# Performance work log

Measured on AMD Instinct MI355X. Metric: run time of the kernel, lower is better.

## Reference

```python
import jax, jax.numpy as jnp
from jax import lax
import numpy as np

B, C, H, W = 32, 256, 16, 16          # batch, planes, feature-map HxW
NBUF, REPS, LAB = 100000, 256, 10     # buffer size, reps dim, label dim
D = REPS + LAB                        # retrieval_data feature dim
DH = 64                               # cross_dim_head (heads=1 -> inner=64)
INNER = DH
EPS = 1e-5


def _ln(x, g, b):
    m = x.mean(-1, keepdims=True)
    v = ((x - m) ** 2).mean(-1, keepdims=True)
    return (x - m) * lax.rsqrt(v + EPS) * g + b


def _conv(x, w):
    return lax.conv_general_dilated(x, w, (1, 1), 'SAME',
                                    dimension_numbers=('NCHW', 'OIHW', 'NCHW'))


def _forward(x, conv1_w, conv2_w, bn1_g, bn1_b, bn2_g, bn2_b, retrieval_data,
             ln_attn_g, ln_attn_b, ln_ctx_g, ln_ctx_b, wq, wk, wv, wqe, wo, bo,
             ln_ff_g, ln_ff_b, w1, b1, w2, b2, topk):
    # eval-mode BatchNorm with running mean=0, var=1
    bn = lambda y, g, b: y * g[None, :, None, None] + b[None, :, None, None]
    out = jax.nn.relu(bn(_conv(x, conv1_w), bn1_g, bn1_b))
    out = bn(_conv(out, conv2_w), bn2_g, bn2_b)
    out = jax.nn.relu(out + x)                        # identity shortcut
    t = out.reshape(B, C, H * W).transpose(0, 2, 1)   # [B, n, C] tokens

    # ---- retrieval cross-attention (PreNorm on x and on context) ----
    xn = _ln(t, ln_attn_g, ln_attn_b)
    ctx = _ln(retrieval_data, ln_ctx_g, ln_ctx_b)     # [NBUF, D]
    q = xn @ wq                                        # [B, n, INNER]
    emb = q @ wqe                                      # [B, n, REPS]
    e0 = emb[:, 0, :]                                  # original loop only uses position 0
    buf_reps = ctx[:, :REPS]                           # [NBUF, REPS]
    # squared L2 has the same ordering as the L2 norm used by torch.topk(largest=False)
    dist2 = jnp.sum((buf_reps[None] - e0[:, None]) ** 2, axis=-1)  # [B, NBUF]
    idx = lax.top_k(-dist2, topk)[1]                   # [B, topk] nearest indices
    retrieved = jnp.take(ctx, idx, axis=0)             # [B, topk, D]; identical for all n positions
    reps_r, labels_r = retrieved[..., :REPS], retrieved[..., REPS:]
    k = reps_r @ wk                                    # reps_for_k: K from reps  [B, topk, INNER]
    v = labels_r @ wv                                  # V from labels            [B, topk, INNER]
    sim = jnp.einsum('bnd,bjd->bnj', q, k) * DH ** -0.5
    attn = jax.nn.softmax(sim, axis=-1)
    o = jnp.einsum('bnj,bjd->bnd', attn, v)
    t = o @ wo + bo + t

    # ---- feed-forward (PreNorm, GEGLU, mult=1) ----
    h = _ln(t, ln_ff_g, ln_ff_b) @ w1 + b1             # [B, n, 2C]
    a, g = jnp.split(h, 2, axis=-1)
    t = (a * jax.nn.gelu(g, approximate=False)) @ w2 + b2 + t

    return t.transpose(0, 2, 1).reshape(B, C, H, W)


def setup_inputs() -> dict:
    key = jax.random.key(0)
    ks = jax.random.split(key, 12)
    s = 0.02
    return {
        'x': jax.random.normal(ks[0], (B, C, H, W), jnp.float32),
        'conv1_w': jax.random.normal(ks[1], (C, C, 3, 3), jnp.float32) * s,
        'conv2_w': jax.random.normal(ks[2], (C, C, 3, 3), jnp.float32) * s,
        'bn1_g': jnp.ones((C,), jnp.float32), 'bn1_b': jnp.zeros((C,), jnp.float32),
        'bn2_g': jnp.ones((C,), jnp.float32), 'bn2_b': jnp.zeros((C,), jnp.float32),
        'retrieval_data': jax.random.normal(ks[3], (NBUF, D), jnp.float32),
        'ln_attn_g': jnp.ones((C,), jnp.float32), 'ln_attn_b': jnp.zeros((C,), jnp.float32),
        'ln_ctx_g': jnp.ones((D,), jnp.float32), 'ln_ctx_b': jnp.zeros((D,), jnp.float32),
        'wq': jax.random.normal(ks[4], (C, INNER), jnp.float32) * s,
        'wk': jax.random.normal(ks[5], (REPS, INNER), jnp.float32) * s,
        'wv': jax.random.normal(ks[6], (LAB, INNER), jnp.float32) * s,
        'wqe': jax.random.normal(ks[7], (INNER, REPS), jnp.float32) * s,
        'wo': jax.random.normal(ks[8], (INNER, C), jnp.float32) * s,
        'bo': jnp.zeros((C,), jnp.float32),
        'ln_ff_g': jnp.ones((C,), jnp.float32), 'ln_ff_b': jnp.zeros((C,), jnp.float32),
        'w1': jax.random.normal(ks[9], (C, 2 * C), jnp.float32) * s,
        'b1': jnp.zeros((2 * C,), jnp.float32),
        'w2': jax.random.normal(ks[10], (C, C), jnp.float32) * s,
        'b2': jnp.zeros((C,), jnp.float32),
        'topk': 32,
    }


def reference(x, conv1_w, conv2_w, bn1_g, bn1_b, bn2_g, bn2_b, retrieval_data,
              ln_attn_g, ln_attn_b, ln_ctx_g, ln_ctx_b, wq, wk, wv, wqe, wo, bo,
              ln_ff_g, ln_ff_b, w1, b1, w2, b2, topk):
    return _forward(x, conv1_w, conv2_w, bn1_g, bn1_b, bn2_g, bn2_b, retrieval_data,
                    ln_attn_g, ln_attn_b, ln_ctx_g, ln_ctx_b, wq, wk, wv, wqe, wo, bo,
                    ln_ff_g, ln_ff_b, w1, b1, w2, b2, topk)
```

## Files before the change

### kernel.cpp

```cpp
#include <hip/hip_runtime.h>
#include <hip/hip_bf16.h>
#include <math.h>

#define DEV __device__ __forceinline__

typedef __attribute__((ext_vector_type(8))) short bf16x8;
typedef __attribute__((ext_vector_type(4))) float f32x4;
typedef __attribute__((ext_vector_type(4))) unsigned int u32x4;
typedef __attribute__((ext_vector_type(2))) unsigned int u32x2;

DEV float b2f(unsigned int u) { return __uint_as_float(u << 16); }
DEV unsigned short f2b(float f) {
    unsigned int x = __float_as_uint(f);
    unsigned int r = x + 0x7fffu + ((x >> 16) & 1u);
    return (unsigned short)(r >> 16);
}
DEV unsigned int pack2(float a, float b) {
    return (unsigned int)f2b(a) | ((unsigned int)f2b(b) << 16);
}
DEV float gelu_exact(float g) {
    return 0.5f * g * (1.f + erff(g * 0.70710678118654752f));
}

constexpr size_t WP1  = 0;
constexpr size_t WP2  = WP1  + 1179648;
constexpr size_t BPQ  = WP2  + 1179648;
constexpr size_t BPO  = BPQ  + 32768;
constexpr size_t BP1  = BPO  + 32768;
constexpr size_t BP2  = BP1  + 262144;
constexpr size_t XTP  = BP2  + 131072;
constexpr size_t O1P  = XTP  + 5308416;
constexpr size_t TBUF = O1P  + 5308416;
constexpr size_t QB   = TBUF + 8388608;
constexpr size_t E0P  = QB   + 1048576;
constexpr size_t DIST = E0P  + 16384;
constexpr size_t CANDV= DIST + 12800000;
constexpr size_t CANDI= CANDV+ 262144;
constexpr size_t IDXB = CANDI+ 262144;
constexpr size_t KBF  = IDXB + 4096;
constexpr size_t VBF  = KBF  + 262144;
constexpr size_t OBF  = VBF  + 262144;
constexpr size_t T2B  = OBF  + 1048576;
constexpr size_t XN2  = T2B  + 8388608;
constexpr size_t UBF  = XN2  + 4194304;

__global__ __launch_bounds__(256) void setup_k(
    const float* __restrict__ x, const float* __restrict__ c1w, const float* __restrict__ c2w,
    const float* __restrict__ wq, const float* __restrict__ wo,
    const float* __restrict__ w1, const float* __restrict__ w2,
    unsigned short* __restrict__ wp1, unsigned short* __restrict__ wp2,
    unsigned short* __restrict__ pq, unsigned short* __restrict__ po,
    unsigned short* __restrict__ p1, unsigned short* __restrict__ p2,
    unsigned short* __restrict__ xtp, unsigned short* __restrict__ o1p)
{
    int blk = blockIdx.x, tid = threadIdx.x;
    if (blk < 576) {
        const float* src = (blk < 288) ? c1w : c2w;
        unsigned short* dst = (blk < 288) ? wp1 : wp2;
        int f = (blk % 288) * 256 + tid;
        int lane = f & 63, s = f >> 6;
        int t = s >> 7, rem = s & 127, kc = rem >> 4, ntg = rem & 15;
        int co = ntg * 16 + (lane & 15);
        int ci0 = kc * 32 + ((lane >> 4) << 3);
        unsigned short v[8];
#pragma unroll
        for (int j = 0; j < 8; ++j) v[j] = f2b(src[((size_t)co * 256 + ci0 + j) * 9 + t]);
        u32x4 q;
        q.x = (unsigned)v[0] | ((unsigned)v[1] << 16);
        q.y = (unsigned)v[2] | ((unsigned)v[3] << 16);
        q.z = (unsigned)v[4] | ((unsigned)v[5] << 16);
        q.w = (unsigned)v[6] | ((unsigned)v[7] << 16);
        *(u32x4*)(dst + (size_t)f * 8) = q;
    } else if (blk < 688) {
        int f = (blk - 576) * 256 + tid;
        const float* src; unsigned short* dst; int NTT, lf;
        if (f < 2048)       { src = wq; dst = pq; NTT = 4;  lf = f; }
        else if (f < 4096)  { src = wo; dst = po; NTT = 16; lf = f - 2048; }
        else if (f < 20480) { src = w1; dst = p1; NTT = 32; lf = f - 4096; }
        else                { src = w2; dst = p2; NTT = 16; lf = f - 20480; }
        int lane = lf & 63, s = lf >> 6;
        int kc = s / NTT, ntg = s % NTT;
        int N = NTT * 16;
        int k0 = kc * 32 + ((lane >> 4) << 3), n = ntg * 16 + (lane & 15);
        unsigned short v[8];
#pragma unroll
        for (int j = 0; j < 8; ++j) v[j] = f2b(src[(size_t)(k0 + j) * N + n]);
        u32x4 q;
        q.x = (unsigned)v[0] | ((unsigned)v[1] << 16);
        q.y = (unsigned)v[2] | ((unsigned)v[3] << 16);
        q.z = (unsigned)v[4] | ((unsigned)v[5] << 16);
        q.w = (unsigned)v[6] | ((unsigned)v[7] << 16);
        *(u32x4*)(dst + (size_t)lf * 8) = q;
    } else {
        int img = blk - 688;
        int h = tid >> 4, w = tid & 15;
        unsigned short* dst = xtp + ((size_t)img * 324 + (h + 1) * 18 + (w + 1)) * 256;
        const float* src = x + (size_t)img * 65536 + tid;
        for (int cc = 0; cc < 8; ++cc) {
            unsigned short v[32];
#pragma unroll
            for (int j = 0; j < 32; ++j) v[j] = f2b(src[(cc * 32 + j) * 256]);
            u32x4* dp = (u32x4*)(dst + cc * 32);
#pragma unroll
            for (int i = 0; i < 4; ++i) {
                u32x4 q;
                q.x = (unsigned)v[i*8+0] | ((unsigned)v[i*8+1] << 16);
                q.y = (unsigned)v[i*8+2] | ((unsigned)v[i*8+3] << 16);
                q.z = (unsigned)v[i*8+4] | ((unsigned)v[i*8+5] << 16);
                q.w = (unsigned)v[i*8+6] | ((unsigned)v[i*8+7] << 16);
                dp[i] = q;
            }
        }
        for (int cell = tid; cell < 324; cell += 256) {
            int hh = cell / 18, ww = cell - hh * 18;
            if (hh == 0 || hh == 17 || ww == 0 || ww == 17) {
                u32x4 z = (u32x4)0u;
                u32x4* zp1 = (u32x4*)(xtp + ((size_t)img * 324 + cell) * 256);
                u32x4* zp2 = (u32x4*)(o1p + ((size_t)img * 324 + cell) * 256);
#pragma unroll
                for (int i = 0; i < 32; ++i) { zp1[i] = z; zp2[i] = z; }
            }
        }
    }
}

template<int EPI>
__global__ __launch_bounds__(256, 2) void conv_mfma(const unsigned short* __restrict__ Asrc,
                                                    const unsigned short* __restrict__ wpack,
                                                    const float* __restrict__ bng,
                                                    const float* __restrict__ bnb,
                                                    const unsigned short* __restrict__ resid,
                                                    unsigned short* __restrict__ outP,
                                                    float* __restrict__ outT)
{
    int blk = blockIdx.x;
    int img = blk >> 4, rem = blk & 15;
    int mo = rem >> 1, nh = rem & 1;
    int tid = threadIdx.x;
    int wv = tid >> 6, lane = tid & 63;
    int lq = lane >> 4, lr = lane & 15;
    int m0 = mo * 32;
    int n0 = nh * 128 + wv * 32;

    f32x4 acc[2][2];
#pragma unroll
    for (int i = 0; i < 2; ++i)
#pragma unroll
        for (int j = 0; j < 2; ++j) acc[i][j] = 0.f;

    int abase[2];
#pragma unroll
    for (int mt = 0; mt < 2; ++mt) {
        int m = m0 + mt * 16 + lr;
        int h = m >> 4, w = m & 15;
        abase[mt] = (img * 324 + (h + 1) * 18 + (w + 1)) * 256 + lq * 8;
    }
    int bb0 = (n0 >> 4) * 512 + lane * 8;

    for (int kc = 0; kc < 8; ++kc) {
#pragma unroll
        for (int tap = 0; tap < 9; ++tap) {
            int dh = tap / 3 - 1, dw = tap % 3 - 1;
            int aoff = (dh * 18 + dw) * 256 + kc * 32;
            bf16x8 a0 = *(const bf16x8*)(Asrc + abase[0] + aoff);
            bf16x8 a1 = *(const bf16x8*)(Asrc + abase[1] + aoff);
            int boff = (tap * 8 + kc) * 8192 + bb0;
            bf16x8 b0 = *(const bf16x8*)(wpack + boff);
            bf16x8 b1 = *(const bf16x8*)(wpack + boff + 512);
            acc[0][0] = __builtin_amdgcn_mfma_f32_16x16x32_bf16(a0, b0, acc[0][0], 0, 0, 0);
            acc[0][1] = __builtin_amdgcn_mfma_f32_16x16x32_bf16(a0, b1, acc[0][1], 0, 0, 0);
            acc[1][0] = __builtin_amdgcn_mfma_f32_16x16x32_bf16(a1, b0, acc[1][0], 0, 0, 0);
            acc[1][1] = __builtin_amdgcn_mfma_f32_16x16x32_bf16(a1, b1, acc[1][1], 0, 0, 0);
        }
    }
#pragma unroll
    for (int nt = 0; nt < 2; ++nt) {
        int co = n0 + nt * 16 + lr;
        float g = bng[co], bb = bnb[co];
#pragma unroll
        for (int mt = 0; mt < 2; ++mt) {
#pragma unroll
            for (int r = 0; r < 4; ++r) {
                int m = m0 + mt * 16 + lq * 4 + r;
                int h = m >> 4, w = m & 15;
                float v = acc[mt][nt][r] * g + bb;
                if (EPI == 0) {
                    v = fmaxf(v, 0.f);
                    outP[((size_t)img * 324 + (h + 1) * 18 + (w + 1)) * 256 + co] = f2b(v);
                } else {
                    v += b2f(resid[((size_t)img * 324 + (h + 1) * 18 + (w + 1)) * 256 + co]);
                    v = fmaxf(v, 0.f);
                    outT[((size_t)img * 256 + m) * 256 + co] = v;
                }
            }
        }
    }
}

__global__ __launch_bounds__(256) void lnq_k(
    const float* __restrict__ t, const float* __restrict__ g, const float* __restrict__ bta,
    const unsigned short* __restrict__ bpq, const float* __restrict__ wqe,
    unsigned short* __restrict__ qb, unsigned short* __restrict__ e0p)
{
    __shared__ __align__(16) unsigned int frag[64 * 132];
    __shared__ float qrow[64];
    int bx = blockIdx.x, tid = threadIdx.x;
    int wv = tid >> 6, lane = tid & 63;
    int c = lane * 4;
    f32x4 gv = *(const f32x4*)(g + c);
    f32x4 bv = *(const f32x4*)(bta + c);
#pragma unroll
    for (int p = 0; p < 16; ++p) {
        int rl = wv * 16 + p;
        f32x4 x = *(const f32x4*)(t + (size_t)(bx * 64 + rl) * 256 + c);
        float s  = x[0] + x[1] + x[2] + x[3];
        float ss = x[0]*x[0] + x[1]*x[1] + x[2]*x[2] + x[3]*x[3];
#pragma unroll
        for (int off = 32; off >= 1; off >>= 1) { s += __shfl_xor(s, off); ss += __shfl_xor(ss, off); }
        float mean = s * (1.f / 256.f);
        float var  = ss * (1.f / 256.f) - mean * mean;
        float rstd = rsqrtf(fmaxf(var, 0.f) + 1e-5f);
        float y0 = (x[0]-mean)*rstd*gv[0] + bv[0];
        float y1 = (x[1]-mean)*rstd*gv[1] + bv[1];
        float y2 = (x[2]-mean)*rstd*gv[2] + bv[2];
        float y3 = (x[3]-mean)*rstd*gv[3] + bv[3];
        frag[rl * 132 + 2 * lane]     = pack2(y0, y1);
        frag[rl * 132 + 2 * lane + 1] = pack2(y2, y3);
    }
    __syncthreads();
    int lq = lane >> 4, lr = lane & 15;
    f32x4 acc[4];
#pragma unroll
    for (int nt = 0; nt < 4; ++nt) acc[nt] = 0.f;
    const short* sA = (const short*)frag;
#pragma unroll
    for (int kc = 0; kc < 8; ++kc) {
        bf16x8 a = *(const bf16x8*)(sA + (wv * 16 + lr) * 264 + kc * 32 + lq * 8);
#pragma unroll
        for (int nt = 0; nt < 4; ++nt) {
            bf16x8 bfr = *(const bf16x8*)(bpq + (size_t)(kc * 4 + nt) * 512 + lane * 8);
            acc[nt] = __builtin_amdgcn_mfma_f32_16x16x32_bf16(a, bfr, acc[nt], 0, 0, 0);
        }
    }
#pragma unroll
    for (int nt = 0; nt < 4; ++nt)
#pragma unroll
        for (int r = 0; r < 4; ++r)
            qb[(size_t)(bx * 64 + wv * 16 + lq * 4 + r) * 64 + nt * 16 + lr] = f2b(acc[nt][r]);
    if ((bx & 3) == 0 && wv == 0 && lq == 0) {
#pragma unroll
        for (int nt = 0; nt < 4; ++nt) qrow[nt * 16 + lr] = acc[nt][0];
    }
    __syncthreads();
    if ((bx & 3) == 0) {
        int b = bx >> 2;
        int r = tid;
        float a2 = 0.f;
#pragma unroll 8
        for (int d = 0; d < 64; ++d) a2 += qrow[d] * wqe[d * 256 + r];
        int nt = b >> 4, kc = r >> 5;
        int ln_ = (b & 15) + (((r >> 3) & 3) << 4);
        int j = r & 7;
        e0p[(((nt * 8 + kc) * 64) + ln_) * 8 + j] = f2b(a2);
    }
}

__global__ __launch_bounds__(256, 4) void lndist_k(
    const float* __restrict__ ctx, const float* __restrict__ lgam, const float* __restrict__ lbet,
    const unsigned short* __restrict__ e0p, float* __restrict__ dist)
{
    __shared__ __align__(16) unsigned int frag[32 * 132];
    __shared__ __align__(16) float rn2s[32];
    int r0 = blockIdx.x * 32;
    int tid = threadIdx.x;
    int wv = tid >> 6, lane = tid & 63;

    float2 d0[8], d1[8], d2[8];
    const float* base = ctx + (size_t)(r0 + wv * 8) * 266;
#pragma unroll
    for (int p = 0; p < 8; ++p) {
        const float* rowp = base + p * 266;
        d0[p] = *(const float2*)(rowp + 2 * lane);
        d1[p] = *(const float2*)(rowp + 128 + 2 * lane);
        if (lane < 5) d2[p] = *(const float2*)(rowp + 256 + 2 * lane);
        else { d2[p].x = 0.f; d2[p].y = 0.f; }
    }
    float2 g0 = *(const float2*)(lgam + 2 * lane);
    float2 g1 = *(const float2*)(lgam + 128 + 2 * lane);
    float2 b0 = *(const float2*)(lbet + 2 * lane);
    float2 b1 = *(const float2*)(lbet + 128 + 2 * lane);

#pragma unroll
    for (int p = 0; p < 8; ++p) {
        int rl = wv * 8 + p;
        float s  = d0[p].x + d0[p].y + d1[p].x + d1[p].y + d2[p].x + d2[p].y;
        float ss = d0[p].x*d0[p].x + d0[p].y*d0[p].y + d1[p].x*d1[p].x + d1[p].y*d1[p].y
                 + d2[p].x*d2[p].x + d2[p].y*d2[p].y;
#pragma unroll
        for (int off = 32; off >= 1; off >>= 1) { s += __shfl_xor(s, off); ss += __shfl_xor(ss, off); }
        float mean = s * (1.f / 266.f);
        float var  = ss * (1.f / 266.f) - mean * mean;
        float rstd = rsqrtf(fmaxf(var, 0.f) + 1e-5f);
        float c0 = (d0[p].x - mean) * rstd * g0.x + b0.x;
        float c1 = (d0[p].y - mean) * rstd * g0.y + b0.y;
        float c2 = (d1[p].x - mean) * rstd * g1.x + b1.x;
        float c3 = (d1[p].y - mean) * rstd * g1.y + b1.y;
        frag[rl * 132 + lane]      = pack2(c0, c1);
        frag[rl * 132 + 64 + lane] = pack2(c2, c3);
        float nsq = c0*c0 + c1*c1 + c2*c2 + c3*c3;
#pragma unroll
        for (int off = 32; off >= 1; off >>= 1) nsq += __shfl_xor(nsq, off);
        if (lane == 0) rn2s[rl] = nsq;
    }
    __syncthreads();

    int lq = lane >> 4, lr = lane & 15;
    int rt = wv & 1, ch = wv >> 1;
    f32x4 acc = 0.f;
    const short* sA = (const short*)frag;
#pragma unroll
    for (int kc = 0; kc < 8; ++kc) {
        bf16x8 a = *(const bf16x8*)(sA + (rt * 16 + lr) * 264 + kc * 32 + lq * 8);
        bf16x8 b = *(const bf16x8*)(e0p + ((ch * 8 + kc) * 64 + lane) * 8);
        acc = __builtin_amdgcn_mfma_f32_16x16x32_bf16(a, b, acc, 0, 0, 0);
    }
    int mbase = r0 + rt * 16 + lq * 4;
    f32x4 rv = *(f32x4*)(rn2s + rt * 16 + lq * 4);
    f32x4 o;
#pragma unroll
    for (int r = 0; r < 4; ++r) o[r] = rv[r] - 2.f * acc[r];
    *(f32x4*)(dist + (size_t)(ch * 16 + lr) * 100000 + mbase) = o;
}

__global__ __launch_bounds__(256) void topk1(const float* __restrict__ dist,
                                             float* __restrict__ candv,
                                             int* __restrict__ candi)
{
    __shared__ float sv[6250];
    __shared__ float wvv[4]; __shared__ int wvi[4];
    int c = blockIdx.x, b = blockIdx.y;
    int tid = threadIdx.x;
    const float* src = dist + (size_t)b * 100000 + c * 6250;
    for (int i = tid; i < 6250; i += 256) sv[i] = src[i];
    __syncthreads();
    for (int it = 0; it < 32; ++it) {
        float lm = 3e38f; int li = 0;
        for (int i = tid; i < 6250; i += 256) {
            float v = sv[i];
            if (v < lm) { lm = v; li = i; }
        }
#pragma unroll
        for (int off = 32; off >= 1; off >>= 1) {
            float ov = __shfl_xor(lm, off);
            int oi = __shfl_xor(li, off);
            if (ov < lm) { lm = ov; li = oi; }
        }
        if ((tid & 63) == 0) { wvv[tid >> 6] = lm; wvi[tid >> 6] = li; }
        __syncthreads();
        if (tid == 0) {
            float m = wvv[0]; int mi = wvi[0];
#pragma unroll
            for (int w = 1; w < 4; ++w) if (wvv[w] < m) { m = wvv[w]; mi = wvi[w]; }
            candv[((size_t)b * 16 + c) * 32 + it] = m;
            candi[((size_t)b * 16 + c) * 32 + it] = c * 6250 + mi;
            sv[mi] = 3e38f;
        }
        __syncthreads();
    }
}

__global__ __launch_bounds__(256) void topk2(const float* __restrict__ candv,
                                             const int* __restrict__ candi,
                                             int* __restrict__ idxo)
{
    __shared__ float sv[512]; __shared__ int si[512];
    __shared__ float wvv[4]; __shared__ int wvi[4];
    int b = blockIdx.x, tid = threadIdx.x;
    for (int i = tid; i < 512; i += 256) { sv[i] = candv[(size_t)b * 512 + i]; si[i] = candi[(size_t)b * 512 + i]; }
    __syncthreads();
    for (int it = 0; it < 32; ++it) {
        float lm = 3e38f; int li = 0;
#pragma unroll
        for (int rep = 0; rep < 2; ++rep) {
            int i = tid + rep * 256;
            float v = sv[i];
            if (v < lm) { lm = v; li = i; }
        }
#pragma unroll
        for (int off = 32; off >= 1; off >>= 1) {
            float ov = __shfl_xor(lm, off);
            int oi = __shfl_xor(li, off);
            if (ov < lm) { lm = ov; li = oi; }
        }
        if ((tid & 63) == 0) { wvv[tid >> 6] = lm; wvi[tid >> 6] = li; }
        __syncthreads();
        if (tid == 0) {
            float m = wvv[0]; int mi = wvi[0];
#pragma unroll
            for (int w = 1; w < 4; ++w) if (wvv[w] < m) { m = wvv[w]; mi = wvi[w]; }
            idxo[b * 32 + it] = si[mi];
            sv[mi] = 3e38f;
        }
        __syncthreads();
    }
}

__global__ __launch_bounds__(64) void gather_kv(const float* __restrict__ ctx,
                                                const float* __restrict__ g,
                                                const float* __restrict__ b,
                                                const int* __restrict__ idxb,
                                                const float* __restrict__ wk,
                                                const float* __restrict__ wvm,
                                                float* __restrict__ kb,
                                                float* __restrict__ vb)
{
    __shared__ float cnv[266];
    int bj = blockIdx.x;
    int lane = threadIdx.x;
    int row = idxb[bj];
    const float* p = ctx + (size_t)row * 266;
    float2 a0 = *(const float2*)(p + 2 * lane);
    float2 a1 = *(const float2*)(p + 128 + 2 * lane);
    float x4 = 0.f, x5 = 0.f;
    if (lane < 5) { float2 a2 = *(const float2*)(p + 256 + 2 * lane); x4 = a2.x; x5 = a2.y; }
    float s  = a0.x + a0.y + a1.x + a1.y + x4 + x5;
    float ss = a0.x*a0.x + a0.y*a0.y + a1.x*a1.x + a1.y*a1.y + x4*x4 + x5*x5;
#pragma unroll
    for (int off = 32; off >= 1; off >>= 1) { s += __shfl_xor(s, off); ss += __shfl_xor(ss, off); }
    float mean = s * (1.f / 266.f);
    float var  = ss * (1.f / 266.f) - mean * mean;
    float rstd = rsqrtf(fmaxf(var, 0.f) + 1e-5f);
    float2 g0 = *(const float2*)(g + 2 * lane);
    float2 g1 = *(const float2*)(g + 128 + 2 * lane);
    float2 b0 = *(const float2*)(b + 2 * lane);
    float2 b1 = *(const float2*)(b + 128 + 2 * lane);
    cnv[2*lane]       = (a0.x - mean) * rstd * g0.x + b0.x;
    cnv[2*lane + 1]   = (a0.y - mean) * rstd * g0.y + b0.y;
    cnv[128 + 2*lane] = (a1.x - mean) * rstd * g1.x + b1.x;
    cnv[129 + 2*lane] = (a1.y - mean) * rstd * g1.y + b1.y;
    if (lane < 5) {
        float2 g2 = *(const float2*)(g + 256 + 2 * lane);
        float2 b2 = *(const float2*)(b + 256 + 2 * lane);
        cnv[256 + 2*lane] = (x4 - mean) * rstd * g2.x + b2.x;
        cnv[257 + 2*lane] = (x5 - mean) * rstd * g2.y + b2.y;
    }
    __syncthreads();
    float acc = 0.f;
#pragma unroll 8
    for (int r = 0; r < 256; ++r) acc += cnv[r] * wk[r * 64 + lane];
    kb[(size_t)bj * 64 + lane] = acc;
    float acc2 = 0.f;
#pragma unroll
    for (int r = 0; r < 10; ++r) acc2 += cnv[256 + r] * wvm[r * 64 + lane];
    vb[(size_t)bj * 64 + lane] = acc2;
}

__global__ __launch_bounds__(256) void attn_k(const unsigned short* __restrict__ q,
                                              const float* __restrict__ kb,
                                              const float* __restrict__ vb,
                                              unsigned short* __restrict__ ob)
{
    __shared__ float kl[32 * 66];
    __shared__ float vl[32 * 66];
    __shared__ float ql[8 * 64];
    __shared__ float pl[8 * 32];
    int b = blockIdx.x >> 5, pxg = blockIdx.x & 31;
    int px_base = pxg * 8;
    int tid = threadIdx.x;

    for (int i = tid; i < 2048; i += 256) {
        int row = i >> 6, d = i & 63;
        kl[row * 66 + d] = kb[(size_t)b * 2048 + i];
        vl[row * 66 + d] = vb[(size_t)b * 2048 + i];
    }
    for (int i = tid; i < 512; i += 256) {
        ql[i] = b2f(q[((size_t)b * 256 + px_base) * 64 + i]);
    }
    __syncthreads();

    int wv = tid >> 6, lane = tid & 63;
    int lp = wv * 2 + (lane >> 5);
    int j = lane & 31;

    const float* qp = ql + lp * 64;
    const float* kp = kl + j * 66;
    float s = 0.f;
#pragma unroll
    for (int d = 0; d < 64; ++d) s += qp[d] * kp[d];
    s *= 0.125f;

    float mx = s;
#pragma unroll
    for (int off = 16; off >= 1; off >>= 1) mx = fmaxf(mx, __shfl_xor(mx, off));
    float p = expf(s - mx);
    float sum = p;
#pragma unroll
    for (int off = 16; off >= 1; off >>= 1) sum += __shfl_xor(sum, off);
    p /= sum;
    pl[lp * 32 + j] = p;

    int d0 = 2 * j;
    float o0 = 0.f, o1 = 0.f;
#pragma unroll
    for (int jj = 0; jj < 32; ++jj) {
        float pj = pl[lp * 32 + jj];
        float2 vv = *(const float2*)(vl + jj * 66 + d0);
        o0 += pj * vv.x;
        o1 += pj * vv.y;
    }
    ((unsigned int*)ob)[(((size_t)b * 256 + px_base + lp) * 64 + d0) >> 1] = pack2(o0, o1);
}

__global__ __launch_bounds__(256) void wo_ln_k(
    const unsigned short* __restrict__ A, const unsigned short* __restrict__ Bp,
    const float* __restrict__ bo, const float* __restrict__ tres,
    float* __restrict__ t2, unsigned short* __restrict__ xn2,
    const float* __restrict__ lng, const float* __restrict__ lnb)
{
    __shared__ __align__(16) float tile[32 * 268];
    int m0 = blockIdx.x * 32;
    int tid = threadIdx.x, wv = tid >> 6, lane = tid & 63, lq = lane >> 4, lr = lane & 15;
    int n0 = wv * 64;
    f32x4 acc[2][4];
#pragma unroll
    for (int i = 0; i < 2; ++i)
#pragma unroll
        for (int j = 0; j < 4; ++j) acc[i][j] = 0.f;
    const unsigned short* a0p = A + (size_t)(m0 + lr) * 64 + lq * 8;
#pragma unroll
    for (int kc = 0; kc < 2; ++kc) {
        bf16x8 a0 = *(const bf16x8*)(a0p + kc * 32);
        bf16x8 a1 = *(const bf16x8*)(a0p + 16 * 64 + kc * 32);
#pragma unroll
        for (int nt = 0; nt < 4; ++nt) {
            bf16x8 bfr = *(const bf16x8*)(Bp + (size_t)(kc * 16 + (n0 >> 4) + nt) * 512 + lane * 8);
            acc[0][nt] = __builtin_amdgcn_mfma_f32_16x16x32_bf16(a0, bfr, acc[0][nt], 0, 0, 0);
            acc[1][nt] = __builtin_amdgcn_mfma_f32_16x16x32_bf16(a1, bfr, acc[1][nt], 0, 0, 0);
        }
    }
#pragma unroll
    for (int mt = 0; mt < 2; ++mt)
#pragma unroll
        for (int nt = 0; nt < 4; ++nt)
#pragma unroll
            for (int r = 0; r < 4; ++r)
                tile[(mt * 16 + lq * 4 + r) * 268 + n0 + nt * 16 + lr] = acc[mt][nt][r];
    __syncthreads();
    int row = tid >> 3, c0 = (tid & 7) * 32;
    const float* trp = tres + (size_t)(m0 + row) * 256 + c0;
    float v[32];
#pragma unroll
    for (int i = 0; i < 8; ++i) {
        f32x4 t4 = *(f32x4*)(tile + row * 268 + c0 + i * 4);
        f32x4 rr = *(const f32x4*)(trp + i * 4);
        f32x4 bb = *(const f32x4*)(bo + c0 + i * 4);
#pragma unroll
        for (int k = 0; k < 4; ++k) v[i*4+k] = t4[k] + rr[k] + bb[k];
    }
    float* t2p = t2 + (size_t)(m0 + row) * 256 + c0;
#pragma unroll
    for (int i = 0; i < 8; ++i) {
        f32x4 o; o[0] = v[i*4]; o[1] = v[i*4+1]; o[2] = v[i*4+2]; o[3] = v[i*4+3];
        *(f32x4*)(t2p + i * 4) = o;
    }
    float s = 0.f, ss = 0.f;
#pragma unroll
    for (int i = 0; i < 32; ++i) { s += v[i]; ss += v[i] * v[i]; }
#pragma unroll
    for (int off = 1; off <= 4; off <<= 1) { s += __shfl_xor(s, off); ss += __shfl_xor(ss, off); }
    float mean = s * (1.f / 256.f);
    float var  = ss * (1.f / 256.f) - mean * mean;
    float rstd = rsqrtf(fmaxf(var, 0.f) + 1e-5f);
    unsigned int pk[16];
#pragma unroll
    for (int i = 0; i < 16; ++i) {
        float y0 = (v[2*i]   - mean) * rstd * lng[c0+2*i]   + lnb[c0+2*i];
        float y1 = (v[2*i+1] - mean) * rstd * lng[c0+2*i+1] + lnb[c0+2*i+1];
        pk[i] = pack2(y0, y1);
    }
    u32x4* dp = (u32x4*)(xn2 + (size_t)(m0 + row) * 256 + c0);
#pragma unroll
    for (int i = 0; i < 4; ++i) {
        u32x4 o; o.x = pk[i*4]; o.y = pk[i*4+1]; o.z = pk[i*4+2]; o.w = pk[i*4+3];
        dp[i] = o;
    }
}

__global__ __launch_bounds__(256) void ff1_k(
    const unsigned short* __restrict__ A, const unsigned short* __restrict__ Bp,
    const float* __restrict__ b1, unsigned short* __restrict__ u)
{
    __shared__ __align__(16) float tile[64 * 68];
    int m0 = blockIdx.x * 64, by = blockIdx.y;
    int tid = threadIdx.x, wv = tid >> 6, lane = tid & 63, lq = lane >> 4, lr = lane & 15;
    int mh = wv & 1, sel = wv >> 1;
    int m0w = m0 + mh * 32;
    int nbase = sel * 256 + by * 32;
    f32x4 acc[2][2];
#pragma unroll
    for (int i = 0; i < 2; ++i)
#pragma unroll
        for (int j = 0; j < 2; ++j) acc[i][j] = 0.f;
    const unsigned short* a0p = A + (size_t)(m0w + lr) * 256 + lq * 8;
#pragma unroll
    for (int kc = 0; kc < 8; ++kc) {
        bf16x8 a0 = *(const bf16x8*)(a0p + kc * 32);
        bf16x8 a1 = *(const bf16x8*)(a0p + 16 * 256 + kc * 32);
#pragma unroll
        for (int nt = 0; nt < 2; ++nt) {
            bf16x8 bfr = *(const bf16x8*)(Bp + (size_t)(kc * 32 + (nbase >> 4) + nt) * 512 + lane * 8);
            acc[0][nt] = __builtin_amdgcn_mfma_f32_16x16x32_bf16(a0, bfr, acc[0][nt], 0, 0, 0);
            acc[1][nt] = __builtin_amdgcn_mfma_f32_16x16x32_bf16(a1, bfr, acc[1][nt], 0, 0, 0);
        }
    }
#pragma unroll
    for (int nt = 0; nt < 2; ++nt) {
        float bias = b1[nbase + nt * 16 + lr];
#pragma unroll
        for (int mt = 0; mt < 2; ++mt)
#pragma unroll
            for (int r = 0; r < 4; ++r)
                tile[(mh * 32 + mt * 16 + lq * 4 + r) * 68 + sel * 32 + nt * 16 + lr] = acc[mt][nt][r] + bias;
    }
    __syncthreads();
    int row = tid >> 2, c0 = (tid & 3) * 8;
    unsigned int pk[4];
#pragma unroll
    for (int i = 0; i < 4; ++i) {
        float a0 = tile[row * 68 + c0 + 2*i];
        float a1 = tile[row * 68 + c0 + 2*i + 1];
        float g0 = tile[row * 68 + 32 + c0 + 2*i];
        float g1 = tile[row * 68 + 32 + c0 + 2*i + 1];
        pk[i] = pack2(a0 * gelu_exact(g0), a1 * gelu_exact(g1));
    }
    u32x4 o; o.x = pk[0]; o.y = pk[1]; o.z = pk[2]; o.w = pk[3];
    *(u32x4*)(u + (size_t)(m0 + row) * 256 + by * 32 + c0) = o;
}

__global__ __launch_bounds__(256) void ff2_k(
    const unsigned short* __restrict__ A, const unsigned short* __restrict__ Bp,
    const float* __restrict__ b2, const float* __restrict__ t2,
    float* __restrict__ out)
{
    __shared__ __align__(16) float tile[64 * 68];
    int m0 = blockIdx.x * 64, n0 = blockIdx.y * 64;
    int tid = threadIdx.x, wv = tid >> 6, lane = tid & 63, lq = lane >> 4, lr = lane & 15;
    int mq = wv & 1, nq = wv >> 1;
    int m0w = m0 + mq * 32, n0w = n0 + nq * 32;
    f32x4 acc[2][2];
#pragma unroll
    for (int i = 0; i < 2; ++i)
#pragma unroll
        for (int j = 0; j < 2; ++j) acc[i][j] = 0.f;
    const unsigned short* a0p = A + (size_t)(m0w + lr) * 256 + lq * 8;
#pragma unroll
    for (int kc = 0; kc < 8; ++kc) {
        bf16x8 a0 = *(const bf16x8*)(a0p + kc * 32);
        bf16x8 a1 = *(const bf16x8*)(a0p + 16 * 256 + kc * 32);
#pragma unroll
        for (int nt = 0; nt < 2; ++nt) {
            bf16x8 bfr = *(const bf16x8*)(Bp + (size_t)(kc * 16 + (n0w >> 4) + nt) * 512 + lane * 8);
            acc[0][nt] = __builtin_amdgcn_mfma_f32_16x16x32_bf16(a0, bfr, acc[0][nt], 0, 0, 0);
            acc[1][nt] = __builtin_amdgcn_mfma_f32_16x16x32_bf16(a1, bfr, acc[1][nt], 0, 0, 0);
        }
    }
#pragma unroll
    for (int nt = 0; nt < 2; ++nt) {
        int col = n0w + nt * 16 + lr;
        float bv = b2[col];
#pragma unroll
        for (int mt = 0; mt < 2; ++mt)
#pragma unroll
            for (int r = 0; r < 4; ++r) {
                int m = m0w + mt * 16 + lq * 4 + r;
                tile[(mq * 32 + mt * 16 + lq * 4 + r) * 68 + nq * 32 + nt * 16 + lr] =
                    acc[mt][nt][r] + bv + t2[(size_t)m * 256 + col];
            }
    }
    __syncthreads();
    int b = m0 >> 8, px0 = m0 & 255;
    int cl = tid >> 2, pc = (tid & 3) * 16;
    float* dp = out + ((size_t)b * 256 + n0 + cl) * 256 + px0 + pc;
#pragma unroll
    for (int i = 0; i < 4; ++i) {
        f32x4 o;
        o[0] = tile[(pc + i * 4 + 0) * 68 + cl];
        o[1] = tile[(pc + i * 4 + 1) * 68 + cl];
        o[2] = tile[(pc + i * 4 + 2) * 68 + cl];
        o[3] = tile[(pc + i * 4 + 3) * 68 + cl];
        *(f32x4*)(dp + i * 4) = o;
    }
}

extern "C" void kernel_launch(void* const* d_in, const int* in_sizes, int n_in,
                              void* d_out, int out_size, void* d_ws, size_t ws_size,
                              hipStream_t stream)
{
    (void)in_sizes; (void)n_in; (void)out_size; (void)ws_size;
    const float* x    = (const float*)d_in[0];
    const float* c1w  = (const float*)d_in[1];
    const float* c2w  = (const float*)d_in[2];
    const float* bn1g = (const float*)d_in[3];
    const float* bn1b = (const float*)d_in[4];
    const float* bn2g = (const float*)d_in[5];
    const float* bn2b = (const float*)d_in[6];
    const float* rdat = (const float*)d_in[7];
    const float* lag  = (const float*)d_in[8];
    const float* labp = (const float*)d_in[9];
    const float* lcg  = (const float*)d_in[10];
    const float* lcb  = (const float*)d_in[11];
    const float* wq   = (const float*)d_in[12];
    const float* wk   = (const float*)d_in[13];
    const float* wv   = (const float*)d_in[14];
    const float* wqe  = (const float*)d_in[15];
    const float* wo   = (const float*)d_in[16];
    const float* bo   = (const float*)d_in[17];
    const float* lfg  = (const float*)d_in[18];
    const float* lfb  = (const float*)d_in[19];
    const float* w1   = (const float*)d_in[20];
    const float* b1   = (const float*)d_in[21];
    const float* w2   = (const float*)d_in[22];
    const float* b2   = (const float*)d_in[23];

    char* ws = (char*)d_ws;
    unsigned short* wp1  = (unsigned short*)(ws + WP1);
    unsigned short* wp2  = (unsigned short*)(ws + WP2);
    unsigned short* bpq  = (unsigned short*)(ws + BPQ);
    unsigned short* bpo  = (unsigned short*)(ws + BPO);
    unsigned short* bp1  = (unsigned short*)(ws + BP1);
    unsigned short* bp2  = (unsigned short*)(ws + BP2);
    unsigned short* xtp  = (unsigned short*)(ws + XTP);
    unsigned short* o1p  = (unsigned short*)(ws + O1P);
    float*          tb   = (float*)(ws + TBUF);
    unsigned short* qb   = (unsigned short*)(ws + QB);
    unsigned short* e0p  = (unsigned short*)(ws + E0P);
    float*          dist = (float*)(ws + DIST);
    float*          cdv  = (float*)(ws + CANDV);
    int*            cdi  = (int*)(ws + CANDI);
    int*            idxb = (int*)(ws + IDXB);
    float*          kb   = (float*)(ws + KBF);
    float*          vbuf = (float*)(ws + VBF);
    unsigned short* ob   = (unsigned short*)(ws + OBF);
    float*          t2   = (float*)(ws + T2B);
    unsigned short* xn2  = (unsigned short*)(ws + XN2);
    unsigned short* ub   = (unsigned short*)(ws + UBF);
    float*          outp = (float*)d_out;

    setup_k<<<720, 256, 0, stream>>>(x, c1w, c2w, wq, wo, w1, w2,
                                     wp1, wp2, bpq, bpo, bp1, bp2, xtp, o1p);
    conv_mfma<0><<<512, 256, 0, stream>>>(xtp, wp1, bn1g, bn1b, nullptr, o1p, nullptr);
    conv_mfma<1><<<512, 256, 0, stream>>>(o1p, wp2, bn2g, bn2b, xtp, nullptr, tb);
    lnq_k<<<128, 256, 0, stream>>>(tb, lag, labp, bpq, wqe, qb, e0p);
    lndist_k<<<3125, 256, 0, stream>>>(rdat, lcg, lcb, e0p, dist);
    topk1<<<dim3(16, 32), 256, 0, stream>>>(dist, cdv, cdi);
    topk2<<<32, 256, 0, stream>>>(cdv, cdi, idxb);
    gather_kv<<<1024, 64, 0, stream>>>(rdat, lcg, lcb, idxb, wk, wv, kb, vbuf);
    attn_k<<<1024, 256, 0, stream>>>(qb, kb, vbuf, ob);
    wo_ln_k<<<256, 256, 0, stream>>>(ob, bpo, bo, tb, t2, xn2, lfg, lfb);
    ff1_k<<<dim3(128, 8), 256, 0, stream>>>(xn2, bp1, b1, ub);
    ff2_k<<<dim3(128, 4), 256, 0, stream>>>(ub, bp2, b2, t2, outp);
}
```

Measured before the change: 461.8 us.

## Enlarge per-wave conv register tile to 64x64 and split input transpose across blocks

The conv kernels now launch one 64-lane wave per block, and each wave computes a 64x64 output tile (4x4 MFMA tiles) instead of four waves each computing 32x32. The aim is more register reuse of the A and B fragments loaded from global memory per MFMA. The input transpose in setup is split into 8 channel-chunk blocks per image, adding 224 blocks, to raise parallelism. The conv grid stays at 512 blocks but holds only 512 waves, so occupancy and latency hiding drop and register pressure rises.

```diff
diff --git a/kernel.cpp b/kernel.cpp
--- a/kernel.cpp
+++ b/kernel.cpp
@@ -92,65 +92,63 @@
         q.w = (unsigned)v[6] | ((unsigned)v[7] << 16);
         *(u32x4*)(dst + (size_t)lf * 8) = q;
     } else {
-        int img = blk - 688;
+        int t = blk - 688;
+        int img = t >> 3, cc = t & 7;
         int h = tid >> 4, w = tid & 15;
-        unsigned short* dst = xtp + ((size_t)img * 324 + (h + 1) * 18 + (w + 1)) * 256;
-        const float* src = x + (size_t)img * 65536 + tid;
-        for (int cc = 0; cc < 8; ++cc) {
-            unsigned short v[32];
-#pragma unroll
-            for (int j = 0; j < 32; ++j) v[j] = f2b(src[(cc * 32 + j) * 256]);
-            u32x4* dp = (u32x4*)(dst + cc * 32);
-#pragma unroll
-            for (int i = 0; i < 4; ++i) {
-                u32x4 q;
-                q.x = (unsigned)v[i*8+0] | ((unsigned)v[i*8+1] << 16);
-                q.y = (unsigned)v[i*8+2] | ((unsigned)v[i*8+3] << 16);
-                q.z = (unsigned)v[i*8+4] | ((unsigned)v[i*8+5] << 16);
-                q.w = (unsigned)v[i*8+6] | ((unsigned)v[i*8+7] << 16);
-                dp[i] = q;
-            }
+        unsigned short* dst = xtp + ((size_t)img * 324 + (h + 1) * 18 + (w + 1)) * 256 + cc * 32;
+        const float* src = x + (size_t)img * 65536 + (size_t)cc * 32 * 256 + tid;
+        unsigned short v[32];
+#pragma unroll
+        for (int j = 0; j < 32; ++j) v[j] = f2b(src[j * 256]);
+        u32x4* dp = (u32x4*)dst;
+#pragma unroll
+        for (int i = 0; i < 4; ++i) {
+            u32x4 q;
+            q.x = (unsigned)v[i*8+0] | ((unsigned)v[i*8+1] << 16);
+            q.y = (unsigned)v[i*8+2] | ((unsigned)v[i*8+3] << 16);
+            q.z = (unsigned)v[i*8+4] | ((unsigned)v[i*8+5] << 16);
+            q.w = (unsigned)v[i*8+6] | ((unsigned)v[i*8+7] << 16);
+            dp[i] = q;
         }
         for (int cell = tid; cell < 324; cell += 256) {
             int hh = cell / 18, ww = cell - hh * 18;
             if (hh == 0 || hh == 17 || ww == 0 || ww == 17) {
                 u32x4 z = (u32x4)0u;
-                u32x4* zp1 = (u32x4*)(xtp + ((size_t)img * 324 + cell) * 256);
-                u32x4* zp2 = (u32x4*)(o1p + ((size_t)img * 324 + cell) * 256);
-#pragma unroll
-                for (int i = 0; i < 32; ++i) { zp1[i] = z; zp2[i] = z; }
+                u32x4* zp1 = (u32x4*)(xtp + ((size_t)img * 324 + cell) * 256 + cc * 32);
+                u32x4* zp2 = (u32x4*)(o1p + ((size_t)img * 324 + cell) * 256 + cc * 32);
+#pragma unroll
+                for (int i = 0; i < 4; ++i) { zp1[i] = z; zp2[i] = z; }
             }
         }
     }
 }
 
 template<int EPI>
-__global__ __launch_bounds__(256, 2) void conv_mfma(const unsigned short* __restrict__ Asrc,
-                                                    const unsigned short* __restrict__ wpack,
-                                                    const float* __restrict__ bng,
-                                                    const float* __restrict__ bnb,
-                                                    const unsigned short* __restrict__ resid,
-                                                    unsigned short* __restrict__ outP,
-                                                    float* __restrict__ outT)
+__global__ __launch_bounds__(64) void conv_mfma(const unsigned short* __restrict__ Asrc,
+                                                const unsigned short* __restrict__ wpack,
+                                                const float* __restrict__ bng,
+                                                const float* __restrict__ bnb,
+                                                const unsigned short* __restrict__ resid,
+                                                unsigned short* __restrict__ outP,
+                                                float* __restrict__ outT)
 {
     int blk = blockIdx.x;
     int img = blk >> 4, rem = blk & 15;
-    int mo = rem >> 1, nh = rem & 1;
-    int tid = threadIdx.x;
-    int wv = tid >> 6, lane = tid & 63;
+    int mo = rem >> 2, nq = rem & 3;
+    int lane = threadIdx.x;
     int lq = lane >> 4, lr = lane & 15;
-    int m0 = mo * 32;
-    int n0 = nh * 128 + wv * 32;
-
-    f32x4 acc[2][2];
-#pragma unroll
-    for (int i = 0; i < 2; ++i)
-#pragma unroll
-        for (int j = 0; j < 2; ++j) acc[i][j] = 0.f;
-
-    int abase[2];
-#pragma unroll
-    for (int mt = 0; mt < 2; ++mt) {
+    int m0 = mo * 64;
+    int n0 = nq * 64;
+
+    f32x4 acc[4][4];
+#pragma unroll
+    for (int i = 0; i < 4; ++i)
+#pragma unroll
+        for (int j = 0; j < 4; ++j) acc[i][j] = 0.f;
+
+    int abase[4];
+#pragma unroll
+    for (int mt = 0; mt < 4; ++mt) {
         int m = m0 + mt * 16 + lr;
         int h = m >> 4, w = m & 15;
         abase[mt] = (img * 324 + (h + 1) * 18 + (w + 1)) * 256 + lq * 8;
@@ -162,23 +160,25 @@
         for (int tap = 0; tap < 9; ++tap) {
             int dh = tap / 3 - 1, dw = tap % 3 - 1;
             int aoff = (dh * 18 + dw) * 256 + kc * 32;
-            bf16x8 a0 = *(const bf16x8*)(Asrc + abase[0] + aoff);
-            bf16x8 a1 = *(const bf16x8*)(Asrc + abase[1] + aoff);
+            bf16x8 a[4], b[4];
+#pragma unroll
+            for (int mt = 0; mt < 4; ++mt) a[mt] = *(const bf16x8*)(Asrc + abase[mt] + aoff);
             int boff = (tap * 8 + kc) * 8192 + bb0;
-            bf16x8 b0 = *(const bf16x8*)(wpack + boff);
-            bf16x8 b1 = *(const bf16x8*)(wpack + boff + 512);
-            acc[0][0] = __builtin_amdgcn_mfma_f32_16x16x32_bf16(a0, b0, acc[0][0], 0, 0, 0);
-            acc[0][1] = __builtin_amdgcn_mfma_f32_16x16x32_bf16(a0, b1, acc[0][1], 0, 0, 0);
-            acc[1][0] = __builtin_amdgcn_mfma_f32_16x16x32_bf16(a1, b0, acc[1][0], 0, 0, 0);
-            acc[1][1] = __builtin_amdgcn_mfma_f32_16x16x32_bf16(a1, b1, acc[1][1], 0, 0, 0);
-        }
-    }
-#pragma unroll
-    for (int nt = 0; nt < 2; ++nt) {
+#pragma unroll
+            for (int nt = 0; nt < 4; ++nt) b[nt] = *(const bf16x8*)(wpack + boff + nt * 512);
+#pragma unroll
+            for (int mt = 0; mt < 4; ++mt)
+#pragma unroll
+                for (int nt = 0; nt < 4; ++nt)
+                    acc[mt][nt] = __builtin_amdgcn_mfma_f32_16x16x32_bf16(a[mt], b[nt], acc[mt][nt], 0, 0, 0);
+        }
+    }
+#pragma unroll
+    for (int nt = 0; nt < 4; ++nt) {
         int co = n0 + nt * 16 + lr;
         float g = bng[co], bb = bnb[co];
 #pragma unroll
-        for (int mt = 0; mt < 2; ++mt) {
+        for (int mt = 0; mt < 4; ++mt) {
 #pragma unroll
             for (int r = 0; r < 4; ++r) {
                 int m = m0 + mt * 16 + lq * 4 + r;
@@ -746,10 +746,10 @@
     unsigned short* ub   = (unsigned short*)(ws + UBF);
     float*          outp = (float*)d_out;
 
-    setup_k<<<720, 256, 0, stream>>>(x, c1w, c2w, wq, wo, w1, w2,
+    setup_k<<<944, 256, 0, stream>>>(x, c1w, c2w, wq, wo, w1, w2,
                                      wp1, wp2, bpq, bpo, bp1, bp2, xtp, o1p);
-    conv_mfma<0><<<512, 256, 0, stream>>>(xtp, wp1, bn1g, bn1b, nullptr, o1p, nullptr);
-    conv_mfma<1><<<512, 256, 0, stream>>>(o1p, wp2, bn2g, bn2b, xtp, nullptr, tb);
+    conv_mfma<0><<<512, 64, 0, stream>>>(xtp, wp1, bn1g, bn1b, nullptr, o1p, nullptr);
+    conv_mfma<1><<<512, 64, 0, stream>>>(o1p, wp2, bn2g, bn2b, xtp, nullptr, tb);
     lnq_k<<<128, 256, 0, stream>>>(tb, lag, labp, bpq, wqe, qb, e0p);
     lndist_k<<<3125, 256, 0, stream>>>(rdat, lcg, lcb, e0p, dist);
     topk1<<<dim3(16, 32), 256, 0, stream>>>(dist, cdv, cdi);
```

Measured after the change: 437.7 us. 5.2% less time.
